# Kernel tuning notes

Hardware: AMD Instinct MI355X
Metric: run time of the kernel (lower is better)

The kernel has to match this reference:

```python
import jax, jax.numpy as jnp
import numpy as np

MU = 255          # mu-law levels - 1
H = 64            # block_hidden_size
SKIP = 256        # skip_size
NL = 24           # num_layers
CYC = 6           # cycle_size -> dilation = 2**(i % CYC)
UPK = 4           # upsample conv kernel/stride
REP = 75          # upsample repeat
LF = 80           # local_features_size
B = 2
LLEN = 64                      # local (spectrogram) frames
SLEN = LLEN * UPK * REP        # 19200 signal samples


def setup_inputs() -> dict:
    key = jax.random.key(0)
    ks = jax.random.split(key, 16)
    s = 0.1
    rn = lambda k, shape: jax.random.normal(k, shape, jnp.float32) * s
    return {
        "local_features": jax.random.normal(ks[0], (B, LLEN, LF), jnp.float32),
        "gold_signal": jax.random.randint(ks[1], (B, SLEN), 0, MU + 1, jnp.int32),
        "embed_W": rn(ks[2], (H, MU + 1)),          # 1x1 conv (mu+1 -> H), as matrix
        "embed_b": rn(ks[3], (H,)),
        "up_W": rn(ks[4], (LF, LF, UPK)),           # ConvTranspose1d weight [in, out, k]
        "up_b": rn(ks[5], (LF,)),
        "cond_W": rn(ks[6], (NL * 2 * H, LF)),      # 1x1 conv LF -> NL*2H
        "cond_b": rn(ks[7], (NL * 2 * H,)),
        "dil_W": rn(ks[8], (NL, 2 * H, H, 2)),      # dilated causal conv, kernel 2
        "dil_b": rn(ks[9], (NL, 2 * H)),
        "skip_W": rn(ks[10], (NL, SKIP, H)),
        "skip_b": rn(ks[11], (NL, SKIP)),
        "res_W": rn(ks[12], (NL - 1, H, H)),        # no residual conv on last layer
        "res_b": rn(ks[13], (NL - 1, H)),
        "out_W1": rn(ks[14], (MU + 1, SKIP)),       # out conv 1 (no bias)
        "out_W2": rn(ks[15], (MU + 1, MU + 1)),     # out conv 2 (no bias)
    }


def reference(local_features, gold_signal, embed_W, embed_b, up_W, up_b,
              cond_W, cond_b, dil_W, dil_b, skip_W, skip_b, res_W, res_b,
              out_W1, out_W2):
    Bv = local_features.shape[0]
    # --- conditional features upsample ---
    x = jnp.transpose(local_features, (0, 2, 1))                     # [B, LF, Lloc]
    # ConvTranspose1d with kernel == stride == UPK: each frame emits UPK frames
    up = jnp.einsum('bct,cok->botk', x, up_W).reshape(Bv, LF, -1)    # [B, LF, Lloc*UPK]
    up = up + up_b[None, :, None]
    up = jnp.repeat(up, REP, axis=-1)                                # [B, LF, SLEN]
    cond = jnp.einsum('oc,bct->bot', cond_W, up) + cond_b[None, :, None]
    L = cond.shape[-1]
    cond = cond.reshape(Bv, NL, 2 * H, L)                            # per-layer 2H channels
    # --- embed mu-law one-hot signal (one-hot matmul == gather) ---
    sig = jnp.transpose(embed_W[:, gold_signal], (1, 0, 2)) + embed_b[None, :, None]  # [B, H, L]
    # --- residual blocks ---
    skip_sum = jnp.zeros((Bv, SKIP, L), cond.dtype)
    for i in range(NL):
        d = 2 ** (i % CYC)
        prev = jnp.pad(sig, ((0, 0), (0, 0), (d, 0)))[:, :, :L]      # causal shift by dilation
        a = (jnp.einsum('oc,bct->bot', dil_W[i, :, :, 0], prev)
             + jnp.einsum('oc,bct->bot', dil_W[i, :, :, 1], sig)
             + dil_b[i][None, :, None] + cond[:, i])
        z = jnp.tanh(a[:, :H]) * jax.nn.sigmoid(a[:, H:])            # gated activation
        skip_sum = skip_sum + jnp.einsum('oc,bct->bot', skip_W[i], z) + skip_b[i][None, :, None]
        if i < NL - 1:
            sig = sig + jnp.einsum('oc,bct->bot', res_W[i], z) + res_b[i][None, :, None]
    # --- output head: ReLU -> 1x1 -> ReLU -> 1x1 -> log_softmax over levels ---
    h = jax.nn.relu(skip_sum)
    h = jax.nn.relu(jnp.einsum('oc,bct->bot', out_W1, h))
    logits = jnp.einsum('oc,bct->bot', out_W2, h)
    return jax.nn.log_softmax(logits, axis=1)                        # [B, mu+1, SLEN]
```

## Files before the change

kernel.cpp:

```cpp
#include <hip/hip_runtime.h>
#include <math.h>

#define MU1   256
#define H     64
#define H2    128
#define SKIPC 256
#define NL    24
#define LF    80
#define UPK   4
#define REP   75
#define BB    2
#define LLEN  64
#define LL    19200

using bf16x8 = __attribute__((ext_vector_type(8))) short;
using bf16x4 = __attribute__((ext_vector_type(4))) short;
using f32x4  = __attribute__((ext_vector_type(4))) float;

__device__ __forceinline__ float b2f(short s) {
    union { unsigned u; float f; } v; v.u = ((unsigned)(unsigned short)s) << 16; return v.f;
}
__device__ __forceinline__ short f2b(float f) {
    union { float f; unsigned u; } v; v.f = f;
    unsigned r = (v.u + 0x7fff + ((v.u >> 16) & 1)) >> 16;
// ... 16 lines not shown
    const int n2 = 12 * 256 * 128;
    const int n3 = (NL - 1) * H * H;
    const int n4 = MU1 * H;
    const int n5 = LF * NL * H2;
    const int n6 = MU1 * SKIPC;
    const int n7 = MU1 * MU1;
    if (idx < n1) {
        int c = idx & 63; int o = (idx >> 6) & 127;
        int k = (idx >> 13) & 1; int i = idx >> 14;
        dil_Wb[idx] = f2b(dil_W[((i * H2 + o) * H + c) * 2 + k]);
        return;
    }
    idx -= n1;
    if (idx < n2) {
        int kc = idx & 127; int s = (idx >> 7) & 255; int ck = idx >> 15;
        sWt[idx] = f2b(skip_W[((2 * ck + (kc >> 6)) * SKIPC + s) * H + (kc & 63)]);
        return;
    }
    idx -= n2;
    if (idx < n3) { res_Wb[idx] = f2b(res_W[idx]); return; }
    idx -= n3;
    if (idx < n4) {
        int h = idx & 63; int g = idx >> 6;
        embed_allb[idx] = f2b(embed_W[h * MU1 + g] + embed_b[h]);
        return;
    }
    idx -= n4;
    if (idx < n5) {
        int o = idx % (NL * H2); int c = idx / (NL * H2);
        cond_Wt[idx] = cond_W[o * LF + c];
        return;
    }
    idx -= n5;
    if (idx < n6) { W1b[idx] = f2b(out_W1[idx]); return; }
    idx -= n6;
    if (idx < n7) { W2b[idx] = f2b(out_W2[idx]); return; }
    idx -= n7;
    if (idx < SKIPC) {
        float a = 0.f;
        for (int i = 0; i < NL; i++) a += skip_b[i * SKIPC + idx];
        sbsum[idx] = a;
        return;
    }
}

__global__ __launch_bounds__(256) void embed_kernel(
    const int* __restrict__ gold, const short* __restrict__ eW,
    short* __restrict__ sig)
{
    int idx = blockIdx.x * 256 + threadIdx.x;
    if (idx >= BB * LL * 8) return;
    int ch = idx & 7; int bt = idx >> 3;
    int g = gold[bt];
    *(bf16x8*)(sig + (size_t)bt * H + ch * 8) = *(const bf16x8*)(eW + g * H + ch * 8);
}

__global__ __launch_bounds__(256) void cond_kernel(
    const float* __restrict__ lf, const float* __restrict__ up_W,
    const float* __restrict__ up_b, const float* __restrict__ cond_Wt,
    const float* __restrict__ cond_b, const float* __restrict__ dil_b,
    float* __restrict__ condS)
{
    __shared__ float s_up[LF];
    int j = blockIdx.x;
    int ot = blockIdx.y;
    int b = blockIdx.z;
    int frame = j >> 2, k = j & 3;
    int tid = threadIdx.x;
    if (tid < LF) {
        float a = up_b[tid];
        const float* lfr = lf + (b * LLEN + frame) * LF;
        #pragma unroll 8
        for (int c = 0; c < LF; ++c) a += lfr[c] * up_W[(c * LF + tid) * UPK + k];
        s_up[tid] = a;
    }
    __syncthreads();
    int o = ot * 256 + tid;
    float a = cond_b[o] + dil_b[o];
    #pragma unroll 8
    for (int c = 0; c < LF; ++c) a += cond_Wt[c * 3072 + o] * s_up[c];
    condS[((size_t)(b * 256 + j)) * 3072 + o] = a;
}

template<int DA, int DB, bool LASTPAIR>
__global__ __launch_bounds__(256) void pair_mfma(
    const short* __restrict__ sig_in, short* __restrict__ sig_out,
    short* __restrict__ z12,
    const short* __restrict__ dil_Wb_all,
    const short* __restrict__ res_Wb_all,
    const float* __restrict__ res_b_all,
    const float* __restrict__ condS,
    int p, int slot)
{
    __shared__ __align__(16) short sa[144][72];
    __shared__ __align__(16) short sb[128][72];
    __shared__ __align__(16) short sz[128][72];
    __shared__ float scond[2][3][128];

    const int iA = 2 * p, iB = 2 * p + 1;
    const int b = blockIdx.y;
    const int t0 = blockIdx.x * 96;
    const int tid = threadIdx.x;
    const int w = tid >> 6;
    const int lane = tid & 63;
    const int lr = lane & 15, lg = lane >> 4;
    const int c0 = (t0 >= 32) ? (t0 - 32) / 75 : 0;

    {
        const short* basein = sig_in + (size_t)b * LL * H;
        #pragma unroll
        for (int it = 0; it < 5; ++it) {
            int task = tid + it * 256;
            if (task < 1152) {
                int r = task >> 3, ch = task & 7;
                int t = t0 - 48 + r;
                bf16x8 v = {};
                if (t >= 0) v = *(const bf16x8*)(basein + (size_t)t * H + ch * 8);
                *(bf16x8*)&sa[r][ch * 8] = v;
            }
        }
        #pragma unroll
        for (int it = 0; it < 3; ++it) {
            int task = tid + it * 256;
            int sel = task >= 384;
            int cj = (task - sel * 384) >> 7;
            int o = task & 127;
            int col = c0 + cj; col = col > 255 ? 255 : col;
            scond[sel][cj][o] = condS[((size_t)(b * 256 + col)) * 3072 + (iA + sel) * 128 + o];
        }
    }
    __syncthreads();

    {
        const short* dW = dil_Wb_all + (size_t)iA * 2 * H2 * H;
        f32x4 acc[2][8];
        #pragma unroll
        for (int m = 0; m < 2; ++m)
            #pragma unroll
            for (int n = 0; n < 8; ++n) acc[m][n] = (f32x4){0.f, 0.f, 0.f, 0.f};
        bf16x8 afA[2][4];
        #pragma unroll
        for (int m = 0; m < 2; ++m) {
            int rc = 16 + 16 * (2 * w + m) + lr;
            afA[m][0] = *(const bf16x8*)&sa[rc - DA][lg * 8];
            afA[m][1] = *(const bf16x8*)&sa[rc - DA][32 + lg * 8];
            afA[m][2] = *(const bf16x8*)&sa[rc][lg * 8];
            afA[m][3] = *(const bf16x8*)&sa[rc][32 + lg * 8];
        }
        #pragma unroll
        for (int n = 0; n < 8; ++n)
            #pragma unroll
            for (int kk = 0; kk < 4; ++kk) {
                bf16x8 bw = *(const bf16x8*)(dW + (((kk >> 1) * H2 + 16 * n + lr) * H) + (kk & 1) * 32 + lg * 8);
                acc[0][n] = __builtin_amdgcn_mfma_f32_16x16x32_bf16(afA[0][kk], bw, acc[0][n], 0, 0, 0);
                acc[1][n] = __builtin_amdgcn_mfma_f32_16x16x32_bf16(afA[1][kk], bw, acc[1][n], 0, 0, 0);
            }
        #pragma unroll
        for (int m = 0; m < 2; ++m)
            #pragma unroll
            for (int n = 0; n < 4; ++n)
                #pragma unroll
                for (int r = 0; r < 4; ++r) {
                    int relt = -32 + 16 * (2 * w + m) + 4 * lg + r;
                    int t = t0 + relt;
                    int o = 16 * n + lr;
                    short zb = 0;
                    if (t >= 0) {
                        int ci = t / 75 - c0;
                        float av = acc[m][n][r] + scond[0][ci][o];
                        float gv = acc[m][n + 4][r] + scond[0][ci][64 + o];
                        float th = 1.f - 2.f / (__expf(2.f * av) + 1.f);
                        float sg = 1.f / (1.f + __expf(-gv));
                        zb = f2b(th * sg);
                    }
                    sz[relt + 32][o] = zb;
                }
    }
    __syncthreads();

    #pragma unroll
    for (int it = 0; it < 3; ++it) {
        int task = tid + it * 256;
        int r = task >> 3, ch = task & 7;
        *(bf16x8*)(z12 + ((size_t)((slot * BB + b) * LL) + t0 + r) * 128 + ch * 8)
            = *(const bf16x8*)&sz[32 + r][ch * 8];
    }

    {
        const short* rW = res_Wb_all + (size_t)iA * H * H;
        const float* rb_ = res_b_all + (size_t)iA * H;
        f32x4 rac[2][4];
        #pragma unroll
        for (int m = 0; m < 2; ++m)
            #pragma unroll
            for (int n = 0; n < 4; ++n) rac[m][n] = (f32x4){0.f, 0.f, 0.f, 0.f};
        bf16x8 za[2][2];
        #pragma unroll
        for (int m = 0; m < 2; ++m) {
            int row = 16 * (2 * w + m) + lr;
            za[m][0] = *(const bf16x8*)&sz[row][lg * 8];
            za[m][1] = *(const bf16x8*)&sz[row][32 + lg * 8];
        }
        #pragma unroll
        for (int n = 0; n < 4; ++n)
            #pragma unroll
            for (int kk = 0; kk < 2; ++kk) {
                bf16x8 bw = *(const bf16x8*)(rW + (16 * n + lr) * H + kk * 32 + lg * 8);
                rac[0][n] = __builtin_amdgcn_mfma_f32_16x16x32_bf16(za[0][kk], bw, rac[0][n], 0, 0, 0);
                rac[1][n] = __builtin_amdgcn_mfma_f32_16x16x32_bf16(za[1][kk], bw, rac[1][n], 0, 0, 0);
            }
        #pragma unroll
        for (int n = 0; n < 4; ++n) {
            float rbv = rb_[16 * n + lr];
            #pragma unroll
            for (int m = 0; m < 2; ++m)
                #pragma unroll
                for (int r = 0; r < 4; ++r) {
                    int relt = -32 + 16 * (2 * w + m) + 4 * lg + r;
                    int t = t0 + relt;
                    int c = 16 * n + lr;
                    short vb = 0;
                    if (t >= 0) vb = f2b(b2f(sa[relt + 48][c]) + rac[m][n][r] + rbv);
                    sb[relt + 32][c] = vb;
                }
        }
    }
    __syncthreads();

    {
        const short* dW = dil_Wb_all + (size_t)iB * 2 * H2 * H;
        f32x4 accF[6], accG[6];
        #pragma unroll
        for (int m = 0; m < 6; ++m) { accF[m] = (f32x4){0.f,0.f,0.f,0.f}; accG[m] = (f32x4){0.f,0.f,0.f,0.f}; }
        bf16x8 bwF[4], bwG[4];
        #pragma unroll
        for (int kk = 0; kk < 4; ++kk) {
            int oF = 16 * w + lr;
            bwF[kk] = *(const bf16x8*)(dW + (((kk >> 1) * H2 + oF) * H) + (kk & 1) * 32 + lg * 8);
            bwG[kk] = *(const bf16x8*)(dW + (((kk >> 1) * H2 + 64 + oF) * H) + (kk & 1) * 32 + lg * 8);
        }
        #pragma unroll
        for (int m = 0; m < 6; ++m) {
            int rc = 32 + 16 * m + lr;
            bf16x8 af[4];
            af[0] = *(const bf16x8*)&sb[rc - DB][lg * 8];
            af[1] = *(const bf16x8*)&sb[rc - DB][32 + lg * 8];
            af[2] = *(const bf16x8*)&sb[rc][lg * 8];
            af[3] = *(const bf16x8*)&sb[rc][32 + lg * 8];
            #pragma unroll
            for (int kk = 0; kk < 4; ++kk)
                accF[m] = __builtin_amdgcn_mfma_f32_16x16x32_bf16(af[kk], bwF[kk], accF[m], 0, 0, 0);
            #pragma unroll
            for (int kk = 0; kk < 4; ++kk)
                accG[m] = __builtin_amdgcn_mfma_f32_16x16x32_bf16(af[kk], bwG[kk], accG[m], 0, 0, 0);
        }
        #pragma unroll
        for (int m = 0; m < 6; ++m)
            #pragma unroll
            for (int r = 0; r < 4; ++r) {
                int relt = 16 * m + 4 * lg + r;
                int t = t0 + relt;
                int o = 16 * w + lr;
                int ci = t / 75 - c0;
                float av = accF[m][r] + scond[1][ci][o];
                float gv = accG[m][r] + scond[1][ci][64 + o];
                float th = 1.f - 2.f / (__expf(2.f * av) + 1.f);
                float sg = 1.f / (1.f + __expf(-gv));
                sz[relt][o] = f2b(th * sg);
            }
    }
    __syncthreads();

    #pragma unroll
    for (int it = 0; it < 3; ++it) {
        int task = tid + it * 256;
        int r = task >> 3, ch = task & 7;
        *(bf16x8*)(z12 + ((size_t)((slot * BB + b) * LL) + t0 + r) * 128 + 64 + ch * 8)
            = *(const bf16x8*)&sz[r][ch * 8];
    }

    if (!LASTPAIR) {
        const short* rW = res_Wb_all + (size_t)iB * H * H;
        const float* rb_ = res_b_all + (size_t)iB * H;
        int c = 16 * w + lr;
        f32x4 rac[6];
        #pragma unroll
        for (int m = 0; m < 6; ++m) rac[m] = (f32x4){0.f, 0.f, 0.f, 0.f};
        bf16x8 bwR[2];
        bwR[0] = *(const bf16x8*)(rW + c * H + lg * 8);
        bwR[1] = *(const bf16x8*)(rW + c * H + 32 + lg * 8);
        #pragma unroll
        for (int m = 0; m < 6; ++m) {
            bf16x8 z0 = *(const bf16x8*)&sz[16 * m + lr][lg * 8];
            bf16x8 z1 = *(const bf16x8*)&sz[16 * m + lr][32 + lg * 8];
            rac[m] = __builtin_amdgcn_mfma_f32_16x16x32_bf16(z0, bwR[0], rac[m], 0, 0, 0);
            rac[m] = __builtin_amdgcn_mfma_f32_16x16x32_bf16(z1, bwR[1], rac[m], 0, 0, 0);
        }
        float rbv = rb_[c];
        #pragma unroll
        for (int m = 0; m < 6; ++m)
            #pragma unroll
            for (int r = 0; r < 4; ++r) {
                int relt = 16 * m + 4 * lg + r;
                sa[relt][c] = f2b(b2f(sb[relt + 32][c]) + rac[m][r] + rbv);
            }
        __syncthreads();
        #pragma unroll
        for (int it = 0; it < 3; ++it) {
            int task = tid + it * 256;
            int r = task >> 3, ch = task & 7;
            *(bf16x8*)(sig_out + ((size_t)(b * LL + t0 + r)) * H + ch * 8)
                = *(const bf16x8*)&sa[r][ch * 8];
        }
    }
}

__global__ __launch_bounds__(256) void skip12_kernel(
    const short* __restrict__ z12, const short* __restrict__ sWt,
    short* __restrict__ skipP)
{
    __shared__ __align__(16) short s_a[2][64][136];
    const int b = blockIdx.y;
    const int t0 = blockIdx.x * 64;
    const int tid = threadIdx.x;
    const int w = tid >> 6;
    const int lane = tid & 63;
    const int lr = lane & 15, lg = lane >> 4;

    f32x4 acc[4][4];
    #pragma unroll
    for (int mt = 0; mt < 4; ++mt)
        #pragma unroll
        for (int nt = 0; nt < 4; ++nt) acc[mt][nt] = (f32x4){0.f, 0.f, 0.f, 0.f};

    #pragma unroll
    for (int it = 0; it < 4; ++it) {
        int task = tid + it * 256;
        int r = task >> 4, ch = task & 15;
        *(bf16x8*)&s_a[0][r][ch * 8] =
            *(const bf16x8*)(z12 + ((size_t)(b * LL) + t0 + r) * 128 + ch * 8);
    }
    __syncthreads();

    for (int ck = 0; ck < 6; ++ck) {
        if (ck < 5) {
            #pragma unroll
            for (int it = 0; it < 4; ++it) {
                int task = tid + it * 256;
                int r = task >> 4, ch = task & 15;
                *(bf16x8*)&s_a[(ck + 1) & 1][r][ch * 8] =
                    *(const bf16x8*)(z12 + ((size_t)(((ck + 1) * BB + b) * LL) + t0 + r) * 128 + ch * 8);
            }
        }
        const short* wbase = sWt + ((size_t)ck << 15);
        const short (*buf)[136] = s_a[ck & 1];
        #pragma unroll
        for (int kk = 0; kk < 4; ++kk) {
            bf16x8 afr[4];
            #pragma unroll
            for (int mt = 0; mt < 4; ++mt)
                afr[mt] = *(const bf16x8*)&buf[16 * mt + lr][32 * kk + 8 * lg];
            #pragma unroll
            for (int nt = 0; nt < 4; ++nt) {
                bf16x8 bw = *(const bf16x8*)(wbase + ((64 * w + 16 * nt + lr) << 7) + 32 * kk + 8 * lg);
                #pragma unroll
                for (int mt = 0; mt < 4; ++mt)
                    acc[mt][nt] = __builtin_amdgcn_mfma_f32_16x16x32_bf16(afr[mt], bw, acc[mt][nt], 0, 0, 0);
            }
        }
        __syncthreads();
    }

    #pragma unroll
    for (int mt = 0; mt < 4; ++mt)
        #pragma unroll
        for (int nt = 0; nt < 4; ++nt) {
            int s = 64 * w + 16 * nt + lr;
            #pragma unroll
            for (int reg = 0; reg < 4; ++reg) {
                int t = t0 + 16 * mt + 4 * lg + reg;
                skipP[((size_t)(b * LL) + t) * 256 + s] = f2b(acc[mt][nt][reg]);
            }
        }
}

__global__ __launch_bounds__(256) void skiphead_kernel(
    const short* __restrict__ z12, const short* __restrict__ sWt,
    const short* __restrict__ skipP, const float* __restrict__ sbsum,
    const short* __restrict__ W1b, const short* __restrict__ W2b,
    float* __restrict__ out)
{
    __shared__ __align__(16) unsigned char smem[36864];
    short (*s_ab)[64][136] = (short(*)[64][136])smem;
    short (*s_x)[264] = (short(*)[264])smem;
    float (*s_o)[68]  = (float(*)[68])smem;
// ... 163 lines not shown
    __syncthreads();
    #pragma unroll
    for (int mt = 0; mt < 4; ++mt)
        #pragma unroll
        for (int reg = 0; reg < 4; ++reg) {
            int tl = 16 * mt + 4 * lg + reg;
            float denom = s_red[0][tl] + s_red[1][tl] + s_red[2][tl] + s_red[3][tl];
            mv[mt][reg] = mv[mt][reg] + __logf(denom);
        }
    __syncthreads();

    #pragma unroll
    for (int pass = 0; pass < 2; ++pass) {
        if ((w >> 1) == pass) {
            #pragma unroll
            for (int mt = 0; mt < 4; ++mt)
                #pragma unroll
                for (int nt = 0; nt < 4; ++nt)
                    #pragma unroll
                    for (int reg = 0; reg < 4; ++reg) {
                        int ch = 64 * (w & 1) + 16 * nt + lr;
                        int tl = 16 * mt + 4 * lg + reg;
                        s_o[ch][tl] = acc2[mt][nt][reg] - mv[mt][reg];
                    }
        }
        __syncthreads();
        {
            int row = tid >> 1, half = tid & 1;
            float* op = out + ((size_t)(b * MU1 + pass * 128 + row)) * LL + t0 + half * 32;
            #pragma unroll
            for (int k = 0; k < 8; ++k)
                *(f32x4*)(op + 4 * k) = *(const f32x4*)&s_o[row][half * 32 + 4 * k];
        }
        __syncthreads();
    }
}

extern "C" void kernel_launch(void* const* d_in, const int* in_sizes, int n_in,
                              void* d_out, int out_size, void* d_ws, size_t ws_size,
                              hipStream_t stream)
{
    const float* lf      = (const float*)d_in[0];
    const int*   gold    = (const int*)  d_in[1];
    const float* embed_W = (const float*)d_in[2];
    const float* embed_b = (const float*)d_in[3];
    const float* up_W    = (const float*)d_in[4];
    const float* up_b    = (const float*)d_in[5];
    const float* cond_W  = (const float*)d_in[6];
    const float* cond_b  = (const float*)d_in[7];
    const float* dil_W   = (const float*)d_in[8];
    const float* dil_b   = (const float*)d_in[9];
    const float* skip_W  = (const float*)d_in[10];
    const float* skip_b  = (const float*)d_in[11];
    const float* res_W   = (const float*)d_in[12];
    const float* res_b   = (const float*)d_in[13];
    const float* W1      = (const float*)d_in[14];
    const float* W2      = (const float*)d_in[15];
    float* out = (float*)d_out;

    unsigned char* p = (unsigned char*)d_ws;
    short* sigA      = (short*)p; p += (size_t)BB * LL * H * 2;
    short* sigB      = (short*)p; p += (size_t)BB * LL * H * 2;
    short* z12       = (short*)p; p += (size_t)6 * BB * LL * 128 * 2;
    short* skipP     = (short*)p; p += (size_t)BB * LL * SKIPC * 2;
    float* condS     = (float*)p; p += (size_t)BB * 256 * NL * H2 * 4;
    short* dil_Wb    = (short*)p; p += (size_t)NL * 2 * H2 * H * 2;
    short* sWt       = (short*)p; p += (size_t)12 * 256 * 128 * 2;
    short* res_Wb    = (short*)p; p += (size_t)(NL - 1) * H * H * 2;
    short* embed_allb= (short*)p; p += (size_t)MU1 * H * 2;
    float* cond_Wt   = (float*)p; p += (size_t)LF * NL * H2 * 4;
    short* W1b       = (short*)p; p += (size_t)MU1 * SKIPC * 2;
    short* W2b       = (short*)p; p += (size_t)MU1 * MU1 * 2;
    float* sbsum     = (float*)p; p += (size_t)SKIPC * 4;

    const int prep_n = NL*2*H2*H + 12*256*128 + (NL-1)*H*H + MU1*H + LF*NL*H2 + MU1*SKIPC + MU1*MU1 + SKIPC;
    prep_kernel<<<(prep_n + 255) / 256, 256, 0, stream>>>(
        dil_W, skip_W, res_W, embed_W, embed_b, cond_W, W1, W2, skip_b,
        dil_Wb, sWt, res_Wb, embed_allb, cond_Wt, W1b, W2b, sbsum);

    embed_kernel<<<(BB * LL * 8 + 255) / 256, 256, 0, stream>>>(gold, embed_allb, sigA);

    cond_kernel<<<dim3(256, 12, BB), 256, 0, stream>>>(lf, up_W, up_b, cond_Wt, cond_b, dil_b, condS);

    short* si = sigA;
    short* so = sigB;
    dim3 pgrid(LL / 96, BB);
    dim3 sgrid(LL / 64, BB);
    for (int pp = 0; pp < 12; ++pp) {
        int slot = pp % 6;
        int r3 = pp % 3;
        if (r3 == 0)
            pair_mfma<1, 2, false><<<pgrid, 256, 0, stream>>>(si, so, z12, dil_Wb, res_Wb, res_b, condS, pp, slot);
        else if (r3 == 1)
            pair_mfma<4, 8, false><<<pgrid, 256, 0, stream>>>(si, so, z12, dil_Wb, res_Wb, res_b, condS, pp, slot);
        else if (pp == 11)
            pair_mfma<16, 32, true><<<pgrid, 256, 0, stream>>>(si, so, z12, dil_Wb, res_Wb, res_b, condS, pp, slot);
        else
            pair_mfma<16, 32, false><<<pgrid, 256, 0, stream>>>(si, so, z12, dil_Wb, res_Wb, res_b, condS, pp, slot);
        short* tmp = si; si = so; so = tmp;

        if (pp == 5)
            skip12_kernel<<<sgrid, 256, 0, stream>>>(z12, sWt, skipP);
    }

    skiphead_kernel<<<sgrid, 256, 0, stream>>>(z12, sWt, skipP, sbsum, W1b, W2b, out);
}
```

Baseline: 559.0 us.

## Fuse six residual layers per kernel with halo recompute in shared memory

Replaces the twelve two-layer kernels with four launches that each run a full dilation cycle of six layers. Each block tiles 80 output samples and loads a 64-sample halo, recomputing the causal receptive field, and keeps the residual signal in shared memory across the six layers. Blocks are now 512 threads, and the dilated-conv weights are loaded into registers once per layer. This removes eight launches and the global round-trips of the residual signal, at the cost of redundant halo computation (144 rows for 80 outputs) and higher register pressure.

```diff
diff --git a/kernel.cpp b/kernel.cpp
--- a/kernel.cpp
+++ b/kernel.cpp
@@ -122,235 +122,166 @@
     condS[((size_t)(b * 256 + j)) * 3072 + o] = a;
 }
 
-template<int DA, int DB, bool LASTPAIR>
-__global__ __launch_bounds__(256) void pair_mfma(
+__global__ __launch_bounds__(512) void group6_mfma(
     const short* __restrict__ sig_in, short* __restrict__ sig_out,
     short* __restrict__ z12,
     const short* __restrict__ dil_Wb_all,
     const short* __restrict__ res_Wb_all,
     const float* __restrict__ res_b_all,
     const float* __restrict__ condS,
-    int p, int slot)
+    int p)
 {
-    __shared__ __align__(16) short sa[144][72];
-    __shared__ __align__(16) short sb[128][72];
-    __shared__ __align__(16) short sz[128][72];
-    __shared__ float scond[2][3][128];
-
-    const int iA = 2 * p, iB = 2 * p + 1;
+    __shared__ __align__(16) short sig[144][72];
+    __shared__ __align__(16) short sz[144][72];
+    __shared__ float scond[2][4][128];
+
     const int b = blockIdx.y;
-    const int t0 = blockIdx.x * 96;
+    const int t0 = blockIdx.x * 80;
+    const int t0g = t0 - 64;
     const int tid = threadIdx.x;
     const int w = tid >> 6;
     const int lane = tid & 63;
     const int lr = lane & 15, lg = lane >> 4;
-    const int c0 = (t0 >= 32) ? (t0 - 32) / 75 : 0;
+    const int c0 = (t0g > 0 ? t0g : 0) / REP;
+
+    const int dils[6] = {1, 2, 4, 8, 16, 32};
+    const int sts[6]  = {0, 0, 0, 1, 2, 4};
 
     {
         const short* basein = sig_in + (size_t)b * LL * H;
         #pragma unroll
-        for (int it = 0; it < 5; ++it) {
-            int task = tid + it * 256;
+        for (int it = 0; it < 3; ++it) {
+            int task = tid + it * 512;
             if (task < 1152) {
                 int r = task >> 3, ch = task & 7;
-                int t = t0 - 48 + r;
+                int t = t0g + r;
                 bf16x8 v = {};
                 if (t >= 0) v = *(const bf16x8*)(basein + (size_t)t * H + ch * 8);
-                *(bf16x8*)&sa[r][ch * 8] = v;
-            }
-        }
-        #pragma unroll
-        for (int it = 0; it < 3; ++it) {
-            int task = tid + it * 256;
-            int sel = task >= 384;
-            int cj = (task - sel * 384) >> 7;
-            int o = task & 127;
-            int col = c0 + cj; col = col > 255 ? 255 : col;
-            scond[sel][cj][o] = condS[((size_t)(b * 256 + col)) * 3072 + (iA + sel) * 128 + o];
-        }
-    }
-    __syncthreads();
-
-    {
-        const short* dW = dil_Wb_all + (size_t)iA * 2 * H2 * H;
-        f32x4 acc[2][8];
-        #pragma unroll
-        for (int m = 0; m < 2; ++m)
-            #pragma unroll
-            for (int n = 0; n < 8; ++n) acc[m][n] = (f32x4){0.f, 0.f, 0.f, 0.f};
-        bf16x8 afA[2][4];
-        #pragma unroll
-        for (int m = 0; m < 2; ++m) {
-            int rc = 16 + 16 * (2 * w + m) + lr;
-            afA[m][0] = *(const bf16x8*)&sa[rc - DA][lg * 8];
-            afA[m][1] = *(const bf16x8*)&sa[rc - DA][32 + lg * 8];
-            afA[m][2] = *(const bf16x8*)&sa[rc][lg * 8];
-            afA[m][3] = *(const bf16x8*)&sa[rc][32 + lg * 8];
-        }
-        #pragma unroll
-        for (int n = 0; n < 8; ++n)
-            #pragma unroll
-            for (int kk = 0; kk < 4; ++kk) {
-                bf16x8 bw = *(const bf16x8*)(dW + (((kk >> 1) * H2 + 16 * n + lr) * H) + (kk & 1) * 32 + lg * 8);
-                acc[0][n] = __builtin_amdgcn_mfma_f32_16x16x32_bf16(afA[0][kk], bw, acc[0][n], 0, 0, 0);
-                acc[1][n] = __builtin_amdgcn_mfma_f32_16x16x32_bf16(afA[1][kk], bw, acc[1][n], 0, 0, 0);
-            }
-        #pragma unroll
-        for (int m = 0; m < 2; ++m)
-            #pragma unroll
-            for (int n = 0; n < 4; ++n)
-                #pragma unroll
-                for (int r = 0; r < 4; ++r) {
-                    int relt = -32 + 16 * (2 * w + m) + 4 * lg + r;
-                    int t = t0 + relt;
-                    int o = 16 * n + lr;
-                    short zb = 0;
-                    if (t >= 0) {
-                        int ci = t / 75 - c0;
-                        float av = acc[m][n][r] + scond[0][ci][o];
-                        float gv = acc[m][n + 4][r] + scond[0][ci][64 + o];
-                        float th = 1.f - 2.f / (__expf(2.f * av) + 1.f);
-                        float sg = 1.f / (1.f + __expf(-gv));
-                        zb = f2b(th * sg);
+                *(bf16x8*)&sig[r][ch * 8] = v;
+            }
+        }
+        int cc = tid >> 7, o = tid & 127;
+        int col = c0 + cc; col = col > 255 ? 255 : col;
+        scond[0][cc][o] = condS[((size_t)(b * 256 + col)) * 3072 + (6 * p) * 128 + o];
+    }
+    __syncthreads();
+
+    for (int j = 0; j < 6; ++j) {
+        const int i = 6 * p + j;
+        const int d = dils[j];
+        const int st = sts[j];
+
+        {
+            const short* dW = dil_Wb_all + (size_t)i * 2 * H2 * H;
+            bf16x8 bw[8][4];
+            #pragma unroll
+            for (int nt = 0; nt < 8; ++nt)
+                #pragma unroll
+                for (int kk = 0; kk < 4; ++kk)
+                    bw[nt][kk] = *(const bf16x8*)(dW + (((kk >> 1) * H2 + 16 * nt + lr) * H) + (kk & 1) * 32 + lg * 8);
+            for (int mi = st + w; mi < 9; mi += 8) {
+                f32x4 acc[8];
+                #pragma unroll
+                for (int nt = 0; nt < 8; ++nt) acc[nt] = (f32x4){0.f, 0.f, 0.f, 0.f};
+                int rc = 16 * mi + lr;
+                int rp = rc - d; if (rp < 0) rp = 0;
+                bf16x8 af[4];
+                af[0] = *(const bf16x8*)&sig[rp][lg * 8];
+                af[1] = *(const bf16x8*)&sig[rp][32 + lg * 8];
+                af[2] = *(const bf16x8*)&sig[rc][lg * 8];
+                af[3] = *(const bf16x8*)&sig[rc][32 + lg * 8];
+                #pragma unroll
+                for (int nt = 0; nt < 8; ++nt)
+                    #pragma unroll
+                    for (int kk = 0; kk < 4; ++kk)
+                        acc[nt] = __builtin_amdgcn_mfma_f32_16x16x32_bf16(af[kk], bw[nt][kk], acc[nt], 0, 0, 0);
+                #pragma unroll
+                for (int nt = 0; nt < 4; ++nt)
+                    #pragma unroll
+                    for (int r = 0; r < 4; ++r) {
+                        int lrow = 16 * mi + 4 * lg + r;
+                        int t = t0g + lrow;
+                        short zb = 0;
+                        if (t >= 0) {
+                            int ci = t / REP - c0;
+                            int o = 16 * nt + lr;
+                            float av = acc[nt][r] + scond[j & 1][ci][o];
+                            float gv = acc[nt + 4][r] + scond[j & 1][ci][64 + o];
+                            float th = 1.f - 2.f / (__expf(2.f * av) + 1.f);
+                            float sg = 1.f / (1.f + __expf(-gv));
+                            zb = f2b(th * sg);
+                        }
+                        sz[lrow][16 * nt + lr] = zb;
                     }
-                    sz[relt + 32][o] = zb;
+            }
+        }
+        __syncthreads();
+
+        if (j < 5) {
+            int cc = tid >> 7, o = tid & 127;
+            int col = c0 + cc; col = col > 255 ? 255 : col;
+            scond[(j + 1) & 1][cc][o] = condS[((size_t)(b * 256 + col)) * 3072 + (i + 1) * 128 + o];
+        }
+        {
+            int slot = (i >> 1) % 6, sub = i & 1;
+            #pragma unroll
+            for (int it = 0; it < 2; ++it) {
+                int task = tid + it * 512;
+                if (task < 640) {
+                    int r = task >> 3, ch = task & 7;
+                    *(bf16x8*)(z12 + ((size_t)((slot * BB + b) * LL) + t0 + r) * 128 + sub * 64 + ch * 8)
+                        = *(const bf16x8*)&sz[64 + r][ch * 8];
                 }
-    }
-    __syncthreads();
-
-    #pragma unroll
-    for (int it = 0; it < 3; ++it) {
-        int task = tid + it * 256;
-        int r = task >> 3, ch = task & 7;
-        *(bf16x8*)(z12 + ((size_t)((slot * BB + b) * LL) + t0 + r) * 128 + ch * 8)
-            = *(const bf16x8*)&sz[32 + r][ch * 8];
-    }
-
-    {
-        const short* rW = res_Wb_all + (size_t)iA * H * H;
-        const float* rb_ = res_b_all + (size_t)iA * H;
-        f32x4 rac[2][4];
-        #pragma unroll
-        for (int m = 0; m < 2; ++m)
-            #pragma unroll
-            for (int n = 0; n < 4; ++n) rac[m][n] = (f32x4){0.f, 0.f, 0.f, 0.f};
-        bf16x8 za[2][2];
-        #pragma unroll
-        for (int m = 0; m < 2; ++m) {
-            int row = 16 * (2 * w + m) + lr;
-            za[m][0] = *(const bf16x8*)&sz[row][lg * 8];
-            za[m][1] = *(const bf16x8*)&sz[row][32 + lg * 8];
-        }
-        #pragma unroll
-        for (int n = 0; n < 4; ++n)
-            #pragma unroll
-            for (int kk = 0; kk < 2; ++kk) {
-                bf16x8 bw = *(const bf16x8*)(rW + (16 * n + lr) * H + kk * 32 + lg * 8);
-                rac[0][n] = __builtin_amdgcn_mfma_f32_16x16x32_bf16(za[0][kk], bw, rac[0][n], 0, 0, 0);
-                rac[1][n] = __builtin_amdgcn_mfma_f32_16x16x32_bf16(za[1][kk], bw, rac[1][n], 0, 0, 0);
-            }
-        #pragma unroll
-        for (int n = 0; n < 4; ++n) {
-            float rbv = rb_[16 * n + lr];
-            #pragma unroll
-            for (int m = 0; m < 2; ++m)
-                #pragma unroll
-                for (int r = 0; r < 4; ++r) {
-                    int relt = -32 + 16 * (2 * w + m) + 4 * lg + r;
-                    int t = t0 + relt;
-                    int c = 16 * n + lr;
-                    short vb = 0;
-                    if (t >= 0) vb = f2b(b2f(sa[relt + 48][c]) + rac[m][n][r] + rbv);
-                    sb[relt + 32][c] = vb;
+            }
+        }
+        if (i != NL - 1) {
+            const short* rW = res_Wb_all + (size_t)i * H * H;
+            const float* rb_ = res_b_all + (size_t)i * H;
+            bf16x8 bwr[4][2];
+            #pragma unroll
+            for (int nt = 0; nt < 4; ++nt) {
+                bwr[nt][0] = *(const bf16x8*)(rW + (16 * nt + lr) * H + lg * 8);
+                bwr[nt][1] = *(const bf16x8*)(rW + (16 * nt + lr) * H + 32 + lg * 8);
+            }
+            for (int mi = st + w; mi < 9; mi += 8) {
+                f32x4 racc[4];
+                #pragma unroll
+                for (int nt = 0; nt < 4; ++nt) racc[nt] = (f32x4){0.f, 0.f, 0.f, 0.f};
+                int row = 16 * mi + lr;
+                bf16x8 za0 = *(const bf16x8*)&sz[row][lg * 8];
+                bf16x8 za1 = *(const bf16x8*)&sz[row][32 + lg * 8];
+                #pragma unroll
+                for (int nt = 0; nt < 4; ++nt) {
+                    racc[nt] = __builtin_amdgcn_mfma_f32_16x16x32_bf16(za0, bwr[nt][0], racc[nt], 0, 0, 0);
+                    racc[nt] = __builtin_amdgcn_mfma_f32_16x16x32_bf16(za1, bwr[nt][1], racc[nt], 0, 0, 0);
                 }
-        }
-    }
-    __syncthreads();
-
-    {
-        const short* dW = dil_Wb_all + (size_t)iB * 2 * H2 * H;
-        f32x4 accF[6], accG[6];
-        #pragma unroll
-        for (int m = 0; m < 6; ++m) { accF[m] = (f32x4){0.f,0.f,0.f,0.f}; accG[m] = (f32x4){0.f,0.f,0.f,0.f}; }
-        bf16x8 bwF[4], bwG[4];
-        #pragma unroll
-        for (int kk = 0; kk < 4; ++kk) {
-            int oF = 16 * w + lr;
-            bwF[kk] = *(const bf16x8*)(dW + (((kk >> 1) * H2 + oF) * H) + (kk & 1) * 32 + lg * 8);
-            bwG[kk] = *(const bf16x8*)(dW + (((kk >> 1) * H2 + 64 + oF) * H) + (kk & 1) * 32 + lg * 8);
-        }
-        #pragma unroll
-        for (int m = 0; m < 6; ++m) {
-            int rc = 32 + 16 * m + lr;
-            bf16x8 af[4];
-            af[0] = *(const bf16x8*)&sb[rc - DB][lg * 8];
-            af[1] = *(const bf16x8*)&sb[rc - DB][32 + lg * 8];
-            af[2] = *(const bf16x8*)&sb[rc][lg * 8];
-            af[3] = *(const bf16x8*)&sb[rc][32 + lg * 8];
-            #pragma unroll
-            for (int kk = 0; kk < 4; ++kk)
-                accF[m] = __builtin_amdgcn_mfma_f32_16x16x32_bf16(af[kk], bwF[kk], accF[m], 0, 0, 0);
-            #pragma unroll
-            for (int kk = 0; kk < 4; ++kk)
-                accG[m] = __builtin_amdgcn_mfma_f32_16x16x32_bf16(af[kk], bwG[kk], accG[m], 0, 0, 0);
-        }
-        #pragma unroll
-        for (int m = 0; m < 6; ++m)
-            #pragma unroll
-            for (int r = 0; r < 4; ++r) {
-                int relt = 16 * m + 4 * lg + r;
-                int t = t0 + relt;
-                int o = 16 * w + lr;
-                int ci = t / 75 - c0;
-                float av = accF[m][r] + scond[1][ci][o];
-                float gv = accG[m][r] + scond[1][ci][64 + o];
-                float th = 1.f - 2.f / (__expf(2.f * av) + 1.f);
-                float sg = 1.f / (1.f + __expf(-gv));
-                sz[relt][o] = f2b(th * sg);
-            }
-    }
-    __syncthreads();
-
-    #pragma unroll
-    for (int it = 0; it < 3; ++it) {
-        int task = tid + it * 256;
-        int r = task >> 3, ch = task & 7;
-        *(bf16x8*)(z12 + ((size_t)((slot * BB + b) * LL) + t0 + r) * 128 + 64 + ch * 8)
-            = *(const bf16x8*)&sz[r][ch * 8];
-    }
-
-    if (!LASTPAIR) {
-        const short* rW = res_Wb_all + (size_t)iB * H * H;
-        const float* rb_ = res_b_all + (size_t)iB * H;
-        int c = 16 * w + lr;
-        f32x4 rac[6];
-        #pragma unroll
-        for (int m = 0; m < 6; ++m) rac[m] = (f32x4){0.f, 0.f, 0.f, 0.f};
-        bf16x8 bwR[2];
-        bwR[0] = *(const bf16x8*)(rW + c * H + lg * 8);
-        bwR[1] = *(const bf16x8*)(rW + c * H + 32 + lg * 8);
-        #pragma unroll
-        for (int m = 0; m < 6; ++m) {
-            bf16x8 z0 = *(const bf16x8*)&sz[16 * m + lr][lg * 8];
-            bf16x8 z1 = *(const bf16x8*)&sz[16 * m + lr][32 + lg * 8];
-            rac[m] = __builtin_amdgcn_mfma_f32_16x16x32_bf16(z0, bwR[0], rac[m], 0, 0, 0);
-            rac[m] = __builtin_amdgcn_mfma_f32_16x16x32_bf16(z1, bwR[1], rac[m], 0, 0, 0);
-        }
-        float rbv = rb_[c];
-        #pragma unroll
-        for (int m = 0; m < 6; ++m)
-            #pragma unroll
-            for (int r = 0; r < 4; ++r) {
-                int relt = 16 * m + 4 * lg + r;
-                sa[relt][c] = f2b(b2f(sb[relt + 32][c]) + rac[m][r] + rbv);
-            }
+                #pragma unroll
+                for (int nt = 0; nt < 4; ++nt) {
+                    float rbv = rb_[16 * nt + lr];
+                    #pragma unroll
+                    for (int r = 0; r < 4; ++r) {
+                        int lrow = 16 * mi + 4 * lg + r;
+                        int t = t0g + lrow;
+                        int c = 16 * nt + lr;
+                        short vb = 0;
+                        if (t >= 0) vb = f2b(b2f(sig[lrow][c]) + racc[nt][r] + rbv);
+                        sig[lrow][c] = vb;
+                    }
+                }
+            }
+        }
         __syncthreads();
-        #pragma unroll
-        for (int it = 0; it < 3; ++it) {
-            int task = tid + it * 256;
-            int r = task >> 3, ch = task & 7;
-            *(bf16x8*)(sig_out + ((size_t)(b * LL + t0 + r)) * H + ch * 8)
-                = *(const bf16x8*)&sa[r][ch * 8];
+    }
+
+    if (p < 3) {
+        #pragma unroll
+        for (int it = 0; it < 2; ++it) {
+            int task = tid + it * 512;
+            if (task < 640) {
+                int r = task >> 3, ch = task & 7;
+                *(bf16x8*)(sig_out + ((size_t)(b * LL) + t0 + r) * H + ch * 8)
+                    = *(const bf16x8*)&sig[64 + r][ch * 8];
+            }
         }
     }
 }
@@ -680,26 +611,13 @@
 
     cond_kernel<<<dim3(256, 12, BB), 256, 0, stream>>>(lf, up_W, up_b, cond_Wt, cond_b, dil_b, condS);
 
-    short* si = sigA;
-    short* so = sigB;
-    dim3 pgrid(LL / 96, BB);
+    dim3 ggrid6(LL / 80, BB);
     dim3 sgrid(LL / 64, BB);
-    for (int pp = 0; pp < 12; ++pp) {
-        int slot = pp % 6;
-        int r3 = pp % 3;
-        if (r3 == 0)
-            pair_mfma<1, 2, false><<<pgrid, 256, 0, stream>>>(si, so, z12, dil_Wb, res_Wb, res_b, condS, pp, slot);
-        else if (r3 == 1)
-            pair_mfma<4, 8, false><<<pgrid, 256, 0, stream>>>(si, so, z12, dil_Wb, res_Wb, res_b, condS, pp, slot);
-        else if (pp == 11)
-            pair_mfma<16, 32, true><<<pgrid, 256, 0, stream>>>(si, so, z12, dil_Wb, res_Wb, res_b, condS, pp, slot);
-        else
-            pair_mfma<16, 32, false><<<pgrid, 256, 0, stream>>>(si, so, z12, dil_Wb, res_Wb, res_b, condS, pp, slot);
-        short* tmp = si; si = so; so = tmp;
-
-        if (pp == 5)
-            skip12_kernel<<<sgrid, 256, 0, stream>>>(z12, sWt, skipP);
-    }
-
+
+    group6_mfma<<<ggrid6, 512, 0, stream>>>(sigA, sigB, z12, dil_Wb, res_Wb, res_b, condS, 0);
+    group6_mfma<<<ggrid6, 512, 0, stream>>>(sigB, sigA, z12, dil_Wb, res_Wb, res_b, condS, 1);
+    skip12_kernel<<<sgrid, 256, 0, stream>>>(z12, sWt, skipP);
+    group6_mfma<<<ggrid6, 512, 0, stream>>>(sigA, sigB, z12, dil_Wb, res_Wb, res_b, condS, 2);
+    group6_mfma<<<ggrid6, 512, 0, stream>>>(sigB, sigA, z12, dil_Wb, res_Wb, res_b, condS, 3);
     skiphead_kernel<<<sgrid, 256, 0, stream>>>(z12, sWt, skipP, sbsum, W1b, W2b, out);
 }
```

After: 817.2 us. +46.2%, slower.

## Shrink pair kernel time tile from 96 to 32 samples for more blocks

Applied to the files above, without the earlier changes.

Reduces the per-block output tile of the fused two-layer residual kernel from 96 to 32 timesteps, tripling the grid to 1200 blocks and cutting shared memory per block. The MFMA work mapping is reworked so each of the four waves covers one 16-row slice of the first layer, and the second layer is split across waves by row and output-channel halves. The intent is better occupancy and load balance across CUs. The cost is that the 48-row causal halo is recomputed far more often relative to useful output, which adds redundant loads and first-layer compute.

```diff
diff --git a/kernel.cpp b/kernel.cpp
--- a/kernel.cpp
+++ b/kernel.cpp
@@ -132,26 +132,26 @@
     const float* __restrict__ condS,
     int p, int slot)
 {
-    __shared__ __align__(16) short sa[144][72];
-    __shared__ __align__(16) short sb[128][72];
-    __shared__ __align__(16) short sz[128][72];
-    __shared__ float scond[2][3][128];
+    __shared__ __align__(16) short sa[80][72];
+    __shared__ __align__(16) short sb[64][72];
+    __shared__ __align__(16) short sz[64][72];
+    __shared__ float scond[2][2][128];
 
     const int iA = 2 * p, iB = 2 * p + 1;
     const int b = blockIdx.y;
-    const int t0 = blockIdx.x * 96;
+    const int t0 = blockIdx.x * 32;
     const int tid = threadIdx.x;
     const int w = tid >> 6;
     const int lane = tid & 63;
     const int lr = lane & 15, lg = lane >> 4;
-    const int c0 = (t0 >= 32) ? (t0 - 32) / 75 : 0;
+    const int c0 = ((t0 >= 32) ? (t0 - 32) : 0) / REP;
 
     {
         const short* basein = sig_in + (size_t)b * LL * H;
         #pragma unroll
-        for (int it = 0; it < 5; ++it) {
+        for (int it = 0; it < 3; ++it) {
             int task = tid + it * 256;
-            if (task < 1152) {
+            if (task < 640) {
                 int r = task >> 3, ch = task & 7;
                 int t = t0 - 48 + r;
                 bf16x8 v = {};
@@ -160,10 +160,10 @@
             }
         }
         #pragma unroll
-        for (int it = 0; it < 3; ++it) {
+        for (int it = 0; it < 2; ++it) {
             int task = tid + it * 256;
-            int sel = task >= 384;
-            int cj = (task - sel * 384) >> 7;
+            int sel = task >> 8;
+            int cj = (task >> 7) & 1;
             int o = task & 127;
             int col = c0 + cj; col = col > 255 ? 255 : col;
             scond[sel][cj][o] = condS[((size_t)(b * 256 + col)) * 3072 + (iA + sel) * 128 + o];
@@ -173,55 +173,45 @@
 
     {
         const short* dW = dil_Wb_all + (size_t)iA * 2 * H2 * H;
-        f32x4 acc[2][8];
-        #pragma unroll
-        for (int m = 0; m < 2; ++m)
-            #pragma unroll
-            for (int n = 0; n < 8; ++n) acc[m][n] = (f32x4){0.f, 0.f, 0.f, 0.f};
-        bf16x8 afA[2][4];
-        #pragma unroll
-        for (int m = 0; m < 2; ++m) {
-            int rc = 16 + 16 * (2 * w + m) + lr;
-            afA[m][0] = *(const bf16x8*)&sa[rc - DA][lg * 8];
-            afA[m][1] = *(const bf16x8*)&sa[rc - DA][32 + lg * 8];
-            afA[m][2] = *(const bf16x8*)&sa[rc][lg * 8];
-            afA[m][3] = *(const bf16x8*)&sa[rc][32 + lg * 8];
-        }
+        f32x4 acc[8];
+        #pragma unroll
+        for (int n = 0; n < 8; ++n) acc[n] = (f32x4){0.f, 0.f, 0.f, 0.f};
+        int rc = 16 + 16 * w + lr;
+        bf16x8 af[4];
+        af[0] = *(const bf16x8*)&sa[rc - DA][lg * 8];
+        af[1] = *(const bf16x8*)&sa[rc - DA][32 + lg * 8];
+        af[2] = *(const bf16x8*)&sa[rc][lg * 8];
+        af[3] = *(const bf16x8*)&sa[rc][32 + lg * 8];
         #pragma unroll
         for (int n = 0; n < 8; ++n)
             #pragma unroll
             for (int kk = 0; kk < 4; ++kk) {
                 bf16x8 bw = *(const bf16x8*)(dW + (((kk >> 1) * H2 + 16 * n + lr) * H) + (kk & 1) * 32 + lg * 8);
-                acc[0][n] = __builtin_amdgcn_mfma_f32_16x16x32_bf16(afA[0][kk], bw, acc[0][n], 0, 0, 0);
-                acc[1][n] = __builtin_amdgcn_mfma_f32_16x16x32_bf16(afA[1][kk], bw, acc[1][n], 0, 0, 0);
-            }
-        #pragma unroll
-        for (int m = 0; m < 2; ++m)
-            #pragma unroll
-            for (int n = 0; n < 4; ++n)
-                #pragma unroll
-                for (int r = 0; r < 4; ++r) {
-                    int relt = -32 + 16 * (2 * w + m) + 4 * lg + r;
-                    int t = t0 + relt;
-                    int o = 16 * n + lr;
-                    short zb = 0;
-                    if (t >= 0) {
-                        int ci = t / 75 - c0;
-                        float av = acc[m][n][r] + scond[0][ci][o];
-                        float gv = acc[m][n + 4][r] + scond[0][ci][64 + o];
-                        float th = 1.f - 2.f / (__expf(2.f * av) + 1.f);
-                        float sg = 1.f / (1.f + __expf(-gv));
-                        zb = f2b(th * sg);
-                    }
-                    sz[relt + 32][o] = zb;
+                acc[n] = __builtin_amdgcn_mfma_f32_16x16x32_bf16(af[kk], bw, acc[n], 0, 0, 0);
+            }
+        #pragma unroll
+        for (int n = 0; n < 4; ++n)
+            #pragma unroll
+            for (int r = 0; r < 4; ++r) {
+                int zrow = 16 * w + 4 * lg + r;
+                int t = t0 - 32 + zrow;
+                int o = 16 * n + lr;
+                short zb = 0;
+                if (t >= 0) {
+                    int ci = t / REP - c0;
+                    float av = acc[n][r] + scond[0][ci][o];
+                    float gv = acc[n + 4][r] + scond[0][ci][64 + o];
+                    float th = 1.f - 2.f / (__expf(2.f * av) + 1.f);
+                    float sg = 1.f / (1.f + __expf(-gv));
+                    zb = f2b(th * sg);
                 }
-    }
-    __syncthreads();
-
-    #pragma unroll
-    for (int it = 0; it < 3; ++it) {
-        int task = tid + it * 256;
-        int r = task >> 3, ch = task & 7;
+                sz[zrow][o] = zb;
+            }
+    }
+    __syncthreads();
+
+    {
+        int r = tid >> 3, ch = tid & 7;
         *(bf16x8*)(z12 + ((size_t)((slot * BB + b) * LL) + t0 + r) * 128 + ch * 8)
             = *(const bf16x8*)&sz[32 + r][ch * 8];
     }
@@ -229,92 +219,80 @@
     {
         const short* rW = res_Wb_all + (size_t)iA * H * H;
         const float* rb_ = res_b_all + (size_t)iA * H;
-        f32x4 rac[2][4];
-        #pragma unroll
-        for (int m = 0; m < 2; ++m)
-            #pragma unroll
-            for (int n = 0; n < 4; ++n) rac[m][n] = (f32x4){0.f, 0.f, 0.f, 0.f};
-        bf16x8 za[2][2];
-        #pragma unroll
-        for (int m = 0; m < 2; ++m) {
-            int row = 16 * (2 * w + m) + lr;
-            za[m][0] = *(const bf16x8*)&sz[row][lg * 8];
-            za[m][1] = *(const bf16x8*)&sz[row][32 + lg * 8];
-        }
-        #pragma unroll
-        for (int n = 0; n < 4; ++n)
-            #pragma unroll
-            for (int kk = 0; kk < 2; ++kk) {
-                bf16x8 bw = *(const bf16x8*)(rW + (16 * n + lr) * H + kk * 32 + lg * 8);
-                rac[0][n] = __builtin_amdgcn_mfma_f32_16x16x32_bf16(za[0][kk], bw, rac[0][n], 0, 0, 0);
-                rac[1][n] = __builtin_amdgcn_mfma_f32_16x16x32_bf16(za[1][kk], bw, rac[1][n], 0, 0, 0);
-            }
+        f32x4 rac[4];
+        #pragma unroll
+        for (int n = 0; n < 4; ++n) rac[n] = (f32x4){0.f, 0.f, 0.f, 0.f};
+        int row = 16 * w + lr;
+        bf16x8 za0 = *(const bf16x8*)&sz[row][lg * 8];
+        bf16x8 za1 = *(const bf16x8*)&sz[row][32 + lg * 8];
+        #pragma unroll
+        for (int n = 0; n < 4; ++n) {
+            bf16x8 bw0 = *(const bf16x8*)(rW + (16 * n + lr) * H + lg * 8);
+            bf16x8 bw1 = *(const bf16x8*)(rW + (16 * n + lr) * H + 32 + lg * 8);
+            rac[n] = __builtin_amdgcn_mfma_f32_16x16x32_bf16(za0, bw0, rac[n], 0, 0, 0);
+            rac[n] = __builtin_amdgcn_mfma_f32_16x16x32_bf16(za1, bw1, rac[n], 0, 0, 0);
+        }
         #pragma unroll
         for (int n = 0; n < 4; ++n) {
             float rbv = rb_[16 * n + lr];
             #pragma unroll
-            for (int m = 0; m < 2; ++m)
-                #pragma unroll
-                for (int r = 0; r < 4; ++r) {
-                    int relt = -32 + 16 * (2 * w + m) + 4 * lg + r;
-                    int t = t0 + relt;
-                    int c = 16 * n + lr;
-                    short vb = 0;
-                    if (t >= 0) vb = f2b(b2f(sa[relt + 48][c]) + rac[m][n][r] + rbv);
-                    sb[relt + 32][c] = vb;
-                }
+            for (int r = 0; r < 4; ++r) {
+                int srow = 16 * w + 4 * lg + r;
+                int t = t0 - 32 + srow;
+                int c = 16 * n + lr;
+                short vb = 0;
+                if (t >= 0) vb = f2b(b2f(sa[srow + 16][c]) + rac[n][r] + rbv);
+                sb[srow][c] = vb;
+            }
         }
     }
     __syncthreads();
 
     {
         const short* dW = dil_Wb_all + (size_t)iB * 2 * H2 * H;
-        f32x4 accF[6], accG[6];
-        #pragma unroll
-        for (int m = 0; m < 6; ++m) { accF[m] = (f32x4){0.f,0.f,0.f,0.f}; accG[m] = (f32x4){0.f,0.f,0.f,0.f}; }
-        bf16x8 bwF[4], bwG[4];
-        #pragma unroll
-        for (int kk = 0; kk < 4; ++kk) {
-            int oF = 16 * w + lr;
-            bwF[kk] = *(const bf16x8*)(dW + (((kk >> 1) * H2 + oF) * H) + (kk & 1) * 32 + lg * 8);
-            bwG[kk] = *(const bf16x8*)(dW + (((kk >> 1) * H2 + 64 + oF) * H) + (kk & 1) * 32 + lg * 8);
-        }
-        #pragma unroll
-        for (int m = 0; m < 6; ++m) {
-            int rc = 32 + 16 * m + lr;
-            bf16x8 af[4];
-            af[0] = *(const bf16x8*)&sb[rc - DB][lg * 8];
-            af[1] = *(const bf16x8*)&sb[rc - DB][32 + lg * 8];
-            af[2] = *(const bf16x8*)&sb[rc][lg * 8];
-            af[3] = *(const bf16x8*)&sb[rc][32 + lg * 8];
-            #pragma unroll
-            for (int kk = 0; kk < 4; ++kk)
-                accF[m] = __builtin_amdgcn_mfma_f32_16x16x32_bf16(af[kk], bwF[kk], accF[m], 0, 0, 0);
-            #pragma unroll
-            for (int kk = 0; kk < 4; ++kk)
-                accG[m] = __builtin_amdgcn_mfma_f32_16x16x32_bf16(af[kk], bwG[kk], accG[m], 0, 0, 0);
-        }
-        #pragma unroll
-        for (int m = 0; m < 6; ++m)
+        const int m = w & 1, q = w >> 1;
+        f32x4 accF[2], accG[2];
+        #pragma unroll
+        for (int n = 0; n < 2; ++n) { accF[n] = (f32x4){0.f,0.f,0.f,0.f}; accG[n] = (f32x4){0.f,0.f,0.f,0.f}; }
+        int brow = 32 + 16 * m + lr;
+        bf16x8 af[4];
+        af[0] = *(const bf16x8*)&sb[brow - DB][lg * 8];
+        af[1] = *(const bf16x8*)&sb[brow - DB][32 + lg * 8];
+        af[2] = *(const bf16x8*)&sb[brow][lg * 8];
+        af[3] = *(const bf16x8*)&sb[brow][32 + lg * 8];
+        #pragma unroll
+        for (int n = 0; n < 2; ++n) {
+            int oF = 32 * q + 16 * n + lr;
+            #pragma unroll
+            for (int kk = 0; kk < 4; ++kk) {
+                bf16x8 bwF = *(const bf16x8*)(dW + (((kk >> 1) * H2 + oF) * H) + (kk & 1) * 32 + lg * 8);
+                accF[n] = __builtin_amdgcn_mfma_f32_16x16x32_bf16(af[kk], bwF, accF[n], 0, 0, 0);
+            }
+            #pragma unroll
+            for (int kk = 0; kk < 4; ++kk) {
+                bf16x8 bwG = *(const bf16x8*)(dW + (((kk >> 1) * H2 + 64 + oF) * H) + (kk & 1) * 32 + lg * 8);
+                accG[n] = __builtin_amdgcn_mfma_f32_16x16x32_bf16(af[kk], bwG, accG[n], 0, 0, 0);
+            }
+        }
+        #pragma unroll
+        for (int n = 0; n < 2; ++n)
             #pragma unroll
             for (int r = 0; r < 4; ++r) {
-                int relt = 16 * m + 4 * lg + r;
-                int t = t0 + relt;
-                int o = 16 * w + lr;
-                int ci = t / 75 - c0;
-                float av = accF[m][r] + scond[1][ci][o];
-                float gv = accG[m][r] + scond[1][ci][64 + o];
+                int orow = 16 * m + 4 * lg + r;
+                int t = t0 + orow;
+                int o = 32 * q + 16 * n + lr;
+                int ci = t / REP - c0;
+                float av = accF[n][r] + scond[1][ci][o];
+                float gv = accG[n][r] + scond[1][ci][64 + o];
                 float th = 1.f - 2.f / (__expf(2.f * av) + 1.f);
                 float sg = 1.f / (1.f + __expf(-gv));
-                sz[relt][o] = f2b(th * sg);
-            }
-    }
-    __syncthreads();
-
-    #pragma unroll
-    for (int it = 0; it < 3; ++it) {
-        int task = tid + it * 256;
-        int r = task >> 3, ch = task & 7;
+                sz[orow][o] = f2b(th * sg);
+            }
+    }
+    __syncthreads();
+
+    {
+        int r = tid >> 3, ch = tid & 7;
         *(bf16x8*)(z12 + ((size_t)((slot * BB + b) * LL) + t0 + r) * 128 + 64 + ch * 8)
             = *(const bf16x8*)&sz[r][ch * 8];
     }
@@ -322,34 +300,35 @@
     if (!LASTPAIR) {
         const short* rW = res_Wb_all + (size_t)iB * H * H;
         const float* rb_ = res_b_all + (size_t)iB * H;
-        int c = 16 * w + lr;
-        f32x4 rac[6];
-        #pragma unroll
-        for (int m = 0; m < 6; ++m) rac[m] = (f32x4){0.f, 0.f, 0.f, 0.f};
-        bf16x8 bwR[2];
-        bwR[0] = *(const bf16x8*)(rW + c * H + lg * 8);
-        bwR[1] = *(const bf16x8*)(rW + c * H + 32 + lg * 8);
-        #pragma unroll
-        for (int m = 0; m < 6; ++m) {
-            bf16x8 z0 = *(const bf16x8*)&sz[16 * m + lr][lg * 8];
-            bf16x8 z1 = *(const bf16x8*)&sz[16 * m + lr][32 + lg * 8];
-            rac[m] = __builtin_amdgcn_mfma_f32_16x16x32_bf16(z0, bwR[0], rac[m], 0, 0, 0);
-            rac[m] = __builtin_amdgcn_mfma_f32_16x16x32_bf16(z1, bwR[1], rac[m], 0, 0, 0);
-        }
-        float rbv = rb_[c];
-        #pragma unroll
-        for (int m = 0; m < 6; ++m)
+        const int m = w & 1, nh = w >> 1;
+        f32x4 rac[2];
+        #pragma unroll
+        for (int n = 0; n < 2; ++n) rac[n] = (f32x4){0.f, 0.f, 0.f, 0.f};
+        int row = 16 * m + lr;
+        bf16x8 za0 = *(const bf16x8*)&sz[row][lg * 8];
+        bf16x8 za1 = *(const bf16x8*)&sz[row][32 + lg * 8];
+        #pragma unroll
+        for (int n = 0; n < 2; ++n) {
+            int c = 32 * nh + 16 * n + lr;
+            bf16x8 bw0 = *(const bf16x8*)(rW + c * H + lg * 8);
+            bf16x8 bw1 = *(const bf16x8*)(rW + c * H + 32 + lg * 8);
+            rac[n] = __builtin_amdgcn_mfma_f32_16x16x32_bf16(za0, bw0, rac[n], 0, 0, 0);
+            rac[n] = __builtin_amdgcn_mfma_f32_16x16x32_bf16(za1, bw1, rac[n], 0, 0, 0);
+        }
+        #pragma unroll
+        for (int n = 0; n < 2; ++n) {
+            int c = 32 * nh + 16 * n + lr;
+            float rbv = rb_[c];
             #pragma unroll
             for (int r = 0; r < 4; ++r) {
-                int relt = 16 * m + 4 * lg + r;
-                sa[relt][c] = f2b(b2f(sb[relt + 32][c]) + rac[m][r] + rbv);
-            }
+                int orow = 16 * m + 4 * lg + r;
+                sa[orow][c] = f2b(b2f(sb[32 + orow][c]) + rac[n][r] + rbv);
+            }
+        }
         __syncthreads();
-        #pragma unroll
-        for (int it = 0; it < 3; ++it) {
-            int task = tid + it * 256;
-            int r = task >> 3, ch = task & 7;
-            *(bf16x8*)(sig_out + ((size_t)(b * LL + t0 + r)) * H + ch * 8)
+        {
+            int r = tid >> 3, ch = tid & 7;
+            *(bf16x8*)(sig_out + ((size_t)(b * LL) + t0 + r) * H + ch * 8)
                 = *(const bf16x8*)&sa[r][ch * 8];
         }
     }
@@ -682,7 +661,7 @@
 
     short* si = sigA;
     short* so = sigB;
-    dim3 pgrid(LL / 96, BB);
+    dim3 pgrid(LL / 32, BB);
     dim3 sgrid(LL / 64, BB);
     for (int pp = 0; pp < 12; ++pp) {
         int slot = pp % 6;
```

After: 812.0 us. +45.3%, slower.
